# Kernel optimization log

Hardware: AMD Instinct MI355X
Metric: run time of the kernel (lower is better)

Reference implementation:

```python
import jax, jax.numpy as jnp
import numpy as np

N = 100000   # nodes
E = 1000000  # edges
D = 128      # input_dim
H = 128      # hidden_dim
P = 128      # proj_dim


def setup_inputs() -> dict:
    key = jax.random.key(0)
    ks = jax.random.split(key, 12)
    def lin(k, fi, fo):
        return jax.random.normal(k, (fi, fo), jnp.float32) / np.sqrt(fi).astype(np.float32)
    x = jax.random.normal(ks[0], (N, D), jnp.float32)
    edge_index = jax.random.randint(ks[1], (2, E), 0, N, dtype=jnp.int32)
    return {
        "x": x,
        "edge_index": edge_index,
        "W1": lin(ks[2], D, H), "b1": jnp.zeros((H,), jnp.float32),
        "W2": lin(ks[3], H, H), "b2": jnp.zeros((H,), jnp.float32),
        "Wp1": lin(ks[4], H, P), "bp1": jnp.zeros((P,), jnp.float32),
        "prelu_a": jnp.float32(0.25),
        "Wp2": lin(ks[5], P, P), "bp2": jnp.zeros((P,), jnp.float32),
    }


def _gcn_conv(h, W, b, src, dst):
    # PyG GCNConv: h' = D^{-1/2} (A + I) D^{-1/2} (h W) + b
    h = h @ W                                   # [N, H]
    loop = jnp.arange(N, dtype=src.dtype)
    s = jnp.concatenate([src, loop])            # add self-loops
    d = jnp.concatenate([dst, loop])
    deg = jax.ops.segment_sum(jnp.ones(s.shape, h.dtype), d, num_segments=N)
    dinv = jax.lax.rsqrt(jnp.maximum(deg, 1.0))  # deg >= 1 due to self-loops
    norm = dinv[s] * dinv[d]                     # [E+N]
    msg = h[s] * norm[:, None]                   # gather + scale
    return jax.ops.segment_sum(msg, d, num_segments=N) + b


def reference(x, edge_index, W1, b1, W2, b2, Wp1, bp1, prelu_a, Wp2, bp2):
    src, dst = edge_index[0], edge_index[1]
    z = jax.nn.relu(_gcn_conv(x, W1, b1, src, dst))   # dropout p=0 -> identity
    z = jax.nn.relu(_gcn_conv(z, W2, b2, src, dst))
    h = z @ Wp1 + bp1
    h = jnp.where(h > 0, h, prelu_a * h)              # PReLU
    p = h @ Wp2 + bp2
    return (z, p)
```

## Files before the change

### kernel.cpp

```cpp
#include <hip/hip_runtime.h>

typedef __bf16 bf16x8 __attribute__((ext_vector_type(8)));
typedef float  f32x4  __attribute__((ext_vector_type(4)));
typedef unsigned short us8 __attribute__((ext_vector_type(8)));
typedef unsigned short us4 __attribute__((ext_vector_type(4)));

__device__ __forceinline__ float bf2f(unsigned short u) {
    return __builtin_bit_cast(float, (unsigned int)u << 16);
}
__device__ __forceinline__ unsigned short f2bf(float f) {
    return __builtin_bit_cast(unsigned short, (__bf16)f);
}

__global__ void prep_w(const float* __restrict__ W, unsigned short* __restrict__ hiT,
                       unsigned short* __restrict__ loT) {
    int i = blockIdx.x * 256 + threadIdx.x;
    int k = i >> 7;
    int n = i & 127;
    float f = W[i];
    __bf16 h = (__bf16)f;
    __bf16 l = (__bf16)(f - (float)h);
    hiT[n * 128 + k] = __builtin_bit_cast(unsigned short, h);
    loT[n * 128 + k] = __builtin_bit_cast(unsigned short, l);
}

__global__ void to_bf16(const float* __restrict__ in, unsigned short* __restrict__ out, int n4) {
    int i = blockIdx.x * 256 + threadIdx.x;
    if (i < n4) {
        f32x4 v = ((const f32x4*)in)[i];
        us4 o;
        o[0] = f2bf(v[0]); o[1] = f2bf(v[1]); o[2] = f2bf(v[2]); o[3] = f2bf(v[3]);
        ((us4*)out)[i] = o;
    }
}

__global__ void zero_i(int* __restrict__ p, int n) {
    int i = blockIdx.x * 256 + threadIdx.x;
    if (i < n) p[i] = 0;
}

__global__ void count_deg(const int* __restrict__ dst, int* __restrict__ cnt, int E) {
    int e = blockIdx.x * 256 + threadIdx.x;
    if (e < E) atomicAdd(&cnt[dst[e]], 1);
}

__global__ void scanA(const int* __restrict__ cnt, int* __restrict__ rowptr,
                      int* __restrict__ bsum, int N) {
    __shared__ int s[1024];
    int t = threadIdx.x;
    int idx = blockIdx.x * 1024 + t;
    int v = (idx < N) ? cnt[idx] : 0;
    int sum = v;
    s[t] = sum;
    __syncthreads();
    for (int o = 1; o < 1024; o <<= 1) {
        int u = (t >= o) ? s[t - o] : 0;
        __syncthreads();
        sum += u;
        s[t] = sum;
        __syncthreads();
    }
    if (idx < N) rowptr[idx] = sum - v;
    if (t == 1023) bsum[blockIdx.x] = sum;
}

__global__ void scanB(int* __restrict__ bsum, int nb) {
    __shared__ int s[128];
    int t = threadIdx.x;
    int v = (t < nb) ? bsum[t] : 0;
    int sum = v;
    s[t] = sum;
    __syncthreads();
    for (int o = 1; o < 128; o <<= 1) {
        int u = (t >= o) ? s[t - o] : 0;
        __syncthreads();
        sum += u;
        s[t] = sum;
        __syncthreads();
    }
    if (t < nb) bsum[t] = sum - v;
}

__global__ void scanC(int* __restrict__ rowptr, const int* __restrict__ bsum,
                      int* __restrict__ cnt_cursor, float* __restrict__ dinv, int N, int E) {
    int i = blockIdx.x * 256 + threadIdx.x;
    if (i < N) {
        int c = cnt_cursor[i];
        int a = rowptr[i] + bsum[i >> 10];
        rowptr[i] = a;
        cnt_cursor[i] = a;
        dinv[i] = rsqrtf((float)(c + 1));
    }
    if (i == 0) rowptr[N] = E;
}

__global__ void fill_csr(const int* __restrict__ src, const int* __restrict__ dst,
                         int* __restrict__ cursor, int* __restrict__ colsrc, int E) {
    int e = blockIdx.x * 256 + threadIdx.x;
    if (e < E) {
        int d = dst[e];
        int p = atomicAdd(&cursor[d], 1);
        colsrc[p] = src[e];
    }
}

__global__ __launch_bounds__(256) void gemm128s(
    const unsigned short* __restrict__ Ahi, const unsigned short* __restrict__ WhiT,
    const unsigned short* __restrict__ WloT, const float* __restrict__ bias,
    const float* __restrict__ prelu_a, float* __restrict__ Cf,
    unsigned short* __restrict__ Cb, int M, int mode)
{
    __shared__ unsigned short sHi[128 * 136];
    __shared__ unsigned short sLo[128 * 136];
    const int tid = threadIdx.x;

    for (int i = tid; i < 2048; i += 256) {
        int row = i >> 4, seg = i & 15;
        *(us8*)(&sHi[row * 136 + seg * 8]) = *(const us8*)(WhiT + row * 128 + seg * 8);
        *(us8*)(&sLo[row * 136 + seg * 8]) = *(const us8*)(WloT + row * 128 + seg * 8);
    }
    __syncthreads();

    const int lane = tid & 63;
    const int wave = tid >> 6;
    const int lc   = lane & 15;
    const int quad = lane >> 4;
    const int rowBlock = blockIdx.x * 128 + wave * 32;

    f32x4 acc[2][8];
    const f32x4 z4 = {0.f, 0.f, 0.f, 0.f};
#pragma unroll
    for (int rs = 0; rs < 2; ++rs)
#pragma unroll
        for (int t = 0; t < 8; ++t) acc[rs][t] = z4;

#pragma unroll
    for (int ks = 0; ks < 4; ++ks) {
        const int kf = ks * 32 + quad * 8;
        bf16x8 a[2];
#pragma unroll
        for (int rs = 0; rs < 2; ++rs) {
            int r = rowBlock + rs * 16 + lc;
            if (r > M - 1) r = M - 1;
            a[rs] = __builtin_bit_cast(bf16x8, *(const us8*)(Ahi + (size_t)r * 128 + kf));
        }
#pragma unroll
        for (int t = 0; t < 8; ++t) {
            bf16x8 bhi = __builtin_bit_cast(bf16x8, *(const us8*)(&sHi[(t * 16 + lc) * 136 + kf]));
            bf16x8 blo = __builtin_bit_cast(bf16x8, *(const us8*)(&sLo[(t * 16 + lc) * 136 + kf]));
#pragma unroll
            for (int rs = 0; rs < 2; ++rs) {
                acc[rs][t] = __builtin_amdgcn_mfma_f32_16x16x32_bf16(a[rs], bhi, acc[rs][t], 0, 0, 0);
                acc[rs][t] = __builtin_amdgcn_mfma_f32_16x16x32_bf16(a[rs], blo, acc[rs][t], 0, 0, 0);
            }
        }
    }

    float av = (mode == 1) ? prelu_a[0] : 0.f;
#pragma unroll
    for (int t = 0; t < 8; ++t) {
        int gcol = t * 16 + lc;
        float bv = (mode != 0) ? bias[gcol] : 0.f;
#pragma unroll
        for (int rs = 0; rs < 2; ++rs) {
#pragma unroll
            for (int i = 0; i < 4; ++i) {
                int r = rowBlock + rs * 16 + quad * 4 + i;
                if (r < M) {
                    float v = acc[rs][t][i] + bv;
                    if (mode == 1) v = (v > 0.f) ? v : av * v;
                    if (mode == 2) Cf[(size_t)r * 128 + gcol] = v;
                    else           Cb[(size_t)r * 128 + gcol] = f2bf(v);
                }
            }
        }
    }
}

__global__ __launch_bounds__(128) void aggregate(
    const unsigned short* __restrict__ Hhi, const float* __restrict__ dinv,
    const int* __restrict__ rowptr, const int* __restrict__ colsrc,
    const float* __restrict__ bias, float* __restrict__ outF,
    unsigned short* __restrict__ outHi, int N)
{
    const int n = blockIdx.x;
    const int tid = threadIdx.x;
    const int g = tid >> 5;
    const int l = tid & 31;
    const float dn = dinv[n];
    const int beg = rowptr[n], end = rowptr[n + 1];

    f32x4 a0 = {0.f, 0.f, 0.f, 0.f};
    f32x4 a1 = a0;

    int i = beg + g;
    for (; i + 4 < end; i += 8) {
        int s0 = colsrc[i];
        int s1 = colsrc[i + 4];
        float w0 = dinv[s0] * dn;
        float w1 = dinv[s1] * dn;
        us4 h0 = *(const us4*)(Hhi + (size_t)s0 * 128 + l * 4);
        us4 h1 = *(const us4*)(Hhi + (size_t)s1 * 128 + l * 4);
#pragma unroll
        for (int j = 0; j < 4; ++j) a0[j] += w0 * bf2f(h0[j]);
#pragma unroll
        for (int j = 0; j < 4; ++j) a1[j] += w1 * bf2f(h1[j]);
    }
    if (i < end) {
        int s0 = colsrc[i];
        float w0 = dinv[s0] * dn;
        us4 h0 = *(const us4*)(Hhi + (size_t)s0 * 128 + l * 4);
#pragma unroll
        for (int j = 0; j < 4; ++j) a0[j] += w0 * bf2f(h0[j]);
    }

    __shared__ f32x4 red[128];
    red[tid] = a0 + a1;
    __syncthreads();

    if (tid < 32) {
        f32x4 sum = red[tid] + red[32 + tid] + red[64 + tid] + red[96 + tid];
        us4 sh = *(const us4*)(Hhi + (size_t)n * 128 + tid * 4);
        f32x4 b4 = *(const f32x4*)(bias + tid * 4);
        float ws = dn * dn;
        f32x4 v;
        us4 ob;
#pragma unroll
        for (int j = 0; j < 4; ++j) {
            v[j] = fmaxf(sum[j] + ws * bf2f(sh[j]) + b4[j], 0.f);
            ob[j] = f2bf(v[j]);
        }
        if (outF) *(f32x4*)(outF + (size_t)n * 128 + tid * 4) = v;
        *(us4*)(outHi + (size_t)n * 128 + tid * 4) = ob;
    }
}

extern "C" void kernel_launch(void* const* d_in, const int* in_sizes, int n_in,
                              void* d_out, int out_size, void* d_ws, size_t ws_size,
                              hipStream_t stream)
{
    const float* x   = (const float*)d_in[0];
    const int*   ei  = (const int*)d_in[1];
    const float* W1  = (const float*)d_in[2];
    const float* b1  = (const float*)d_in[3];
    const float* W2  = (const float*)d_in[4];
    const float* b2  = (const float*)d_in[5];
    const float* Wp1 = (const float*)d_in[6];
    const float* bp1 = (const float*)d_in[7];
    const float* pa  = (const float*)d_in[8];
    const float* Wp2 = (const float*)d_in[9];
    const float* bp2 = (const float*)d_in[10];

    const int N = in_sizes[0] / 128;
    const int E = in_sizes[1] / 2;
    const int* src = ei;
    const int* dst = ei + E;

    float* outF = (float*)d_out;
    float* zbuf = outF;
    float* pbuf = outF + (size_t)N * 128;

    char* w = (char*)d_ws;
    size_t off = 0;
    auto alloc = [&](size_t bytes) {
        void* p = w + off;
        off = (off + bytes + 255) & ~(size_t)255;
        return p;
    };
    unsigned short* S1 = (unsigned short*)alloc((size_t)N * 128 * sizeof(unsigned short));
    unsigned short* S2 = (unsigned short*)alloc((size_t)N * 128 * sizeof(unsigned short));
    float* dinv   = (float*)alloc((size_t)N * sizeof(float));
    int*   rowptr = (int*)alloc((size_t)(N + 1) * sizeof(int));
    int*   cntcur = (int*)alloc((size_t)N * sizeof(int));
    int*   colsrc = (int*)alloc((size_t)E * sizeof(int));
    int*   bsum   = (int*)alloc(1024);
    unsigned short* wt = (unsigned short*)alloc((size_t)4 * 2 * 128 * 128 * sizeof(unsigned short));
    (void)ws_size; (void)n_in; (void)out_size;

    auto hiP = [&](int m) { return wt + (size_t)m * 2 * 16384; };
    auto loP = [&](int m) { return wt + (size_t)m * 2 * 16384 + 16384; };

    hipLaunchKernelGGL(prep_w, dim3(64), dim3(256), 0, stream, W1,  hiP(0), loP(0));
    hipLaunchKernelGGL(prep_w, dim3(64), dim3(256), 0, stream, W2,  hiP(1), loP(1));
    hipLaunchKernelGGL(prep_w, dim3(64), dim3(256), 0, stream, Wp1, hiP(2), loP(2));
    hipLaunchKernelGGL(prep_w, dim3(64), dim3(256), 0, stream, Wp2, hiP(3), loP(3));

    const int n4 = N * 128 / 4;
    hipLaunchKernelGGL(to_bf16, dim3((n4 + 255) / 256), dim3(256), 0, stream, x, S1, n4);

    const int nb = (N + 1023) >> 10;
    hipLaunchKernelGGL(zero_i,    dim3((N + 255) / 256), dim3(256), 0, stream, cntcur, N);
    hipLaunchKernelGGL(count_deg, dim3((E + 255) / 256), dim3(256), 0, stream, dst, cntcur, E);
    hipLaunchKernelGGL(scanA,     dim3(nb), dim3(1024), 0, stream, cntcur, rowptr, bsum, N);
    hipLaunchKernelGGL(scanB,     dim3(1), dim3(128), 0, stream, bsum, nb);
    hipLaunchKernelGGL(scanC,     dim3((N + 255) / 256), dim3(256), 0, stream, rowptr, bsum, cntcur, dinv, N, E);
    hipLaunchKernelGGL(fill_csr,  dim3((E + 255) / 256), dim3(256), 0, stream, src, dst, cntcur, colsrc, E);

    const int gb = (N + 127) / 128;
    hipLaunchKernelGGL(gemm128s, dim3(gb), dim3(256), 0, stream, S1, hiP(0), loP(0),
                       (const float*)nullptr, (const float*)nullptr, (float*)nullptr, S2, N, 0);
    hipLaunchKernelGGL(aggregate, dim3(N), dim3(128), 0, stream, S2, dinv, rowptr, colsrc,
                       b1, (float*)nullptr, S1, N);
    hipLaunchKernelGGL(gemm128s, dim3(gb), dim3(256), 0, stream, S1, hiP(1), loP(1),
                       (const float*)nullptr, (const float*)nullptr, (float*)nullptr, S2, N, 0);
    hipLaunchKernelGGL(aggregate, dim3(N), dim3(128), 0, stream, S2, dinv, rowptr, colsrc,
                       b2, zbuf, S1, N);
    hipLaunchKernelGGL(gemm128s, dim3(gb), dim3(256), 0, stream, S1, hiP(2), loP(2),
                       bp1, pa, (float*)nullptr, S2, N, 1);
    hipLaunchKernelGGL(gemm128s, dim3(gb), dim3(256), 0, stream, S2, hiP(3), loP(3),
                       bp2, (const float*)nullptr, pbuf, (unsigned short*)nullptr, N, 2);
}
```

Before: 568.9 us.

## Pack edge weights into CSR and aggregate one warp per node

Precomputes each edge's normalization weight during CSR fill and stores it next to the source index as an int2 record, so aggregation no longer gathers dinv per edge. Aggregation now assigns one 32-lane group per destination node (8 nodes per 256-thread block) with a 4-way unrolled edge loop, removing the shared-memory reduction and the block-wide sync. It also merges the four weight-prep launches into one and replaces the zeroing kernel with a memset. In exchange the edge array doubles in size, and load balance now depends on per-node degree within a wavefront.

```diff
diff --git a/kernel.cpp b/kernel.cpp
--- a/kernel.cpp
+++ b/kernel.cpp
@@ -12,16 +12,19 @@
     return __builtin_bit_cast(unsigned short, (__bf16)f);
 }
 
-__global__ void prep_w(const float* __restrict__ W, unsigned short* __restrict__ hiT,
-                       unsigned short* __restrict__ loT) {
+__global__ void prep_w4(const float* __restrict__ W0, const float* __restrict__ W1,
+                        const float* __restrict__ W2, const float* __restrict__ W3,
+                        unsigned short* __restrict__ wt) {
     int i = blockIdx.x * 256 + threadIdx.x;
-    int k = i >> 7;
-    int n = i & 127;
-    float f = W[i];
+    int m = i >> 14, r = i & 16383;
+    const float* W = (m == 0) ? W0 : (m == 1) ? W1 : (m == 2) ? W2 : W3;
+    float f = W[r];
+    int k = r >> 7, n = r & 127;
     __bf16 h = (__bf16)f;
     __bf16 l = (__bf16)(f - (float)h);
-    hiT[n * 128 + k] = __builtin_bit_cast(unsigned short, h);
-    loT[n * 128 + k] = __builtin_bit_cast(unsigned short, l);
+    unsigned short* base = wt + m * 32768;
+    base[n * 128 + k]         = __builtin_bit_cast(unsigned short, h);
+    base[16384 + n * 128 + k] = __builtin_bit_cast(unsigned short, l);
 }
 
 __global__ void to_bf16(const float* __restrict__ in, unsigned short* __restrict__ out, int n4) {
@@ -32,11 +35,6 @@
         o[0] = f2bf(v[0]); o[1] = f2bf(v[1]); o[2] = f2bf(v[2]); o[3] = f2bf(v[3]);
         ((us4*)out)[i] = o;
     }
-}
-
-__global__ void zero_i(int* __restrict__ p, int n) {
-    int i = blockIdx.x * 256 + threadIdx.x;
-    if (i < n) p[i] = 0;
 }
 
 __global__ void count_deg(const int* __restrict__ dst, int* __restrict__ cnt, int E) {
@@ -82,25 +80,34 @@
 }
 
 __global__ void scanC(int* __restrict__ rowptr, const int* __restrict__ bsum,
-                      int* __restrict__ cnt_cursor, float* __restrict__ dinv, int N, int E) {
+                      int* __restrict__ cnt_cursor, float* __restrict__ dinv,
+                      float* __restrict__ selfw, int N, int E) {
     int i = blockIdx.x * 256 + threadIdx.x;
     if (i < N) {
         int c = cnt_cursor[i];
         int a = rowptr[i] + bsum[i >> 10];
         rowptr[i] = a;
         cnt_cursor[i] = a;
-        dinv[i] = rsqrtf((float)(c + 1));
+        float dv = rsqrtf((float)(c + 1));
+        dinv[i] = dv;
+        selfw[i] = dv * dv;
     }
     if (i == 0) rowptr[N] = E;
 }
 
 __global__ void fill_csr(const int* __restrict__ src, const int* __restrict__ dst,
-                         int* __restrict__ cursor, int* __restrict__ colsrc, int E) {
+                         int* __restrict__ cursor, const float* __restrict__ dinv,
+                         int2* __restrict__ epack, int E) {
     int e = blockIdx.x * 256 + threadIdx.x;
     if (e < E) {
+        int s = src[e];
         int d = dst[e];
+        float w = dinv[s] * dinv[d];
         int p = atomicAdd(&cursor[d], 1);
-        colsrc[p] = src[e];
+        int2 rec;
+        rec.x = s;
+        rec.y = __builtin_bit_cast(int, w);
+        epack[p] = rec;
     }
 }
 
@@ -177,62 +184,68 @@
     }
 }
 
-__global__ __launch_bounds__(128) void aggregate(
-    const unsigned short* __restrict__ Hhi, const float* __restrict__ dinv,
-    const int* __restrict__ rowptr, const int* __restrict__ colsrc,
+__global__ __launch_bounds__(256) void aggregate(
+    const unsigned short* __restrict__ Hhi, const float* __restrict__ selfw,
+    const int* __restrict__ rowptr, const int2* __restrict__ epack,
     const float* __restrict__ bias, float* __restrict__ outF,
     unsigned short* __restrict__ outHi, int N)
 {
-    const int n = blockIdx.x;
     const int tid = threadIdx.x;
     const int g = tid >> 5;
     const int l = tid & 31;
-    const float dn = dinv[n];
+    const int n = blockIdx.x * 8 + g;
+    if (n >= N) return;
+
     const int beg = rowptr[n], end = rowptr[n + 1];
+    const size_t fo = (size_t)l * 4;
 
     f32x4 a0 = {0.f, 0.f, 0.f, 0.f};
-    f32x4 a1 = a0;
-
-    int i = beg + g;
-    for (; i + 4 < end; i += 8) {
-        int s0 = colsrc[i];
-        int s1 = colsrc[i + 4];
-        float w0 = dinv[s0] * dn;
-        float w1 = dinv[s1] * dn;
-        us4 h0 = *(const us4*)(Hhi + (size_t)s0 * 128 + l * 4);
-        us4 h1 = *(const us4*)(Hhi + (size_t)s1 * 128 + l * 4);
+    f32x4 a1 = a0, a2 = a0, a3 = a0;
+
+    int i = beg;
+    for (; i + 3 < end; i += 4) {
+        int2 e0 = epack[i];
+        int2 e1 = epack[i + 1];
+        int2 e2 = epack[i + 2];
+        int2 e3 = epack[i + 3];
+        us4 h0 = *(const us4*)(Hhi + (size_t)e0.x * 128 + fo);
+        us4 h1 = *(const us4*)(Hhi + (size_t)e1.x * 128 + fo);
+        us4 h2 = *(const us4*)(Hhi + (size_t)e2.x * 128 + fo);
+        us4 h3 = *(const us4*)(Hhi + (size_t)e3.x * 128 + fo);
+        float w0 = __builtin_bit_cast(float, e0.y);
+        float w1 = __builtin_bit_cast(float, e1.y);
+        float w2 = __builtin_bit_cast(float, e2.y);
+        float w3 = __builtin_bit_cast(float, e3.y);
 #pragma unroll
         for (int j = 0; j < 4; ++j) a0[j] += w0 * bf2f(h0[j]);
 #pragma unroll
         for (int j = 0; j < 4; ++j) a1[j] += w1 * bf2f(h1[j]);
-    }
-    if (i < end) {
-        int s0 = colsrc[i];
-        float w0 = dinv[s0] * dn;
-        us4 h0 = *(const us4*)(Hhi + (size_t)s0 * 128 + l * 4);
+#pragma unroll
+        for (int j = 0; j < 4; ++j) a2[j] += w2 * bf2f(h2[j]);
+#pragma unroll
+        for (int j = 0; j < 4; ++j) a3[j] += w3 * bf2f(h3[j]);
+    }
+    for (; i < end; ++i) {
+        int2 e0 = epack[i];
+        us4 h0 = *(const us4*)(Hhi + (size_t)e0.x * 128 + fo);
+        float w0 = __builtin_bit_cast(float, e0.y);
 #pragma unroll
         for (int j = 0; j < 4; ++j) a0[j] += w0 * bf2f(h0[j]);
     }
 
-    __shared__ f32x4 red[128];
-    red[tid] = a0 + a1;
-    __syncthreads();
-
-    if (tid < 32) {
-        f32x4 sum = red[tid] + red[32 + tid] + red[64 + tid] + red[96 + tid];
-        us4 sh = *(const us4*)(Hhi + (size_t)n * 128 + tid * 4);
-        f32x4 b4 = *(const f32x4*)(bias + tid * 4);
-        float ws = dn * dn;
-        f32x4 v;
-        us4 ob;
-#pragma unroll
-        for (int j = 0; j < 4; ++j) {
-            v[j] = fmaxf(sum[j] + ws * bf2f(sh[j]) + b4[j], 0.f);
-            ob[j] = f2bf(v[j]);
-        }
-        if (outF) *(f32x4*)(outF + (size_t)n * 128 + tid * 4) = v;
-        *(us4*)(outHi + (size_t)n * 128 + tid * 4) = ob;
-    }
+    float sw = selfw[n];
+    us4 sh = *(const us4*)(Hhi + (size_t)n * 128 + fo);
+    f32x4 b4 = *(const f32x4*)(bias + l * 4);
+    f32x4 sum = (a0 + a1) + (a2 + a3);
+    f32x4 v;
+    us4 ob;
+#pragma unroll
+    for (int j = 0; j < 4; ++j) {
+        v[j] = fmaxf(sum[j] + sw * bf2f(sh[j]) + b4[j], 0.f);
+        ob[j] = f2bf(v[j]);
+    }
+    if (outF) *(f32x4*)(outF + (size_t)n * 128 + fo) = v;
+    *(us4*)(outHi + (size_t)n * 128 + fo) = ob;
 }
 
 extern "C" void kernel_launch(void* const* d_in, const int* in_sizes, int n_in,
@@ -270,40 +283,38 @@
     unsigned short* S1 = (unsigned short*)alloc((size_t)N * 128 * sizeof(unsigned short));
     unsigned short* S2 = (unsigned short*)alloc((size_t)N * 128 * sizeof(unsigned short));
     float* dinv   = (float*)alloc((size_t)N * sizeof(float));
+    float* selfw  = (float*)alloc((size_t)N * sizeof(float));
     int*   rowptr = (int*)alloc((size_t)(N + 1) * sizeof(int));
     int*   cntcur = (int*)alloc((size_t)N * sizeof(int));
-    int*   colsrc = (int*)alloc((size_t)E * sizeof(int));
+    int2*  epack  = (int2*)alloc((size_t)E * sizeof(int2));
     int*   bsum   = (int*)alloc(1024);
     unsigned short* wt = (unsigned short*)alloc((size_t)4 * 2 * 128 * 128 * sizeof(unsigned short));
     (void)ws_size; (void)n_in; (void)out_size;
 
-    auto hiP = [&](int m) { return wt + (size_t)m * 2 * 16384; };
-    auto loP = [&](int m) { return wt + (size_t)m * 2 * 16384 + 16384; };
-
-    hipLaunchKernelGGL(prep_w, dim3(64), dim3(256), 0, stream, W1,  hiP(0), loP(0));
-    hipLaunchKernelGGL(prep_w, dim3(64), dim3(256), 0, stream, W2,  hiP(1), loP(1));
-    hipLaunchKernelGGL(prep_w, dim3(64), dim3(256), 0, stream, Wp1, hiP(2), loP(2));
-    hipLaunchKernelGGL(prep_w, dim3(64), dim3(256), 0, stream, Wp2, hiP(3), loP(3));
-
+    auto hiP = [&](int m) { return wt + (size_t)m * 32768; };
+    auto loP = [&](int m) { return wt + (size_t)m * 32768 + 16384; };
+
+    hipLaunchKernelGGL(prep_w4, dim3(256), dim3(256), 0, stream, W1, W2, Wp1, Wp2, wt);
     const int n4 = N * 128 / 4;
     hipLaunchKernelGGL(to_bf16, dim3((n4 + 255) / 256), dim3(256), 0, stream, x, S1, n4);
 
+    hipMemsetAsync(cntcur, 0, (size_t)N * sizeof(int), stream);
     const int nb = (N + 1023) >> 10;
-    hipLaunchKernelGGL(zero_i,    dim3((N + 255) / 256), dim3(256), 0, stream, cntcur, N);
     hipLaunchKernelGGL(count_deg, dim3((E + 255) / 256), dim3(256), 0, stream, dst, cntcur, E);
     hipLaunchKernelGGL(scanA,     dim3(nb), dim3(1024), 0, stream, cntcur, rowptr, bsum, N);
     hipLaunchKernelGGL(scanB,     dim3(1), dim3(128), 0, stream, bsum, nb);
-    hipLaunchKernelGGL(scanC,     dim3((N + 255) / 256), dim3(256), 0, stream, rowptr, bsum, cntcur, dinv, N, E);
-    hipLaunchKernelGGL(fill_csr,  dim3((E + 255) / 256), dim3(256), 0, stream, src, dst, cntcur, colsrc, E);
+    hipLaunchKernelGGL(scanC,     dim3((N + 255) / 256), dim3(256), 0, stream, rowptr, bsum, cntcur, dinv, selfw, N, E);
+    hipLaunchKernelGGL(fill_csr,  dim3((E + 255) / 256), dim3(256), 0, stream, src, dst, cntcur, dinv, epack, E);
 
     const int gb = (N + 127) / 128;
+    const int ab = (N + 7) / 8;
     hipLaunchKernelGGL(gemm128s, dim3(gb), dim3(256), 0, stream, S1, hiP(0), loP(0),
                        (const float*)nullptr, (const float*)nullptr, (float*)nullptr, S2, N, 0);
-    hipLaunchKernelGGL(aggregate, dim3(N), dim3(128), 0, stream, S2, dinv, rowptr, colsrc,
+    hipLaunchKernelGGL(aggregate, dim3(ab), dim3(256), 0, stream, S2, selfw, rowptr, epack,
                        b1, (float*)nullptr, S1, N);
     hipLaunchKernelGGL(gemm128s, dim3(gb), dim3(256), 0, stream, S1, hiP(1), loP(1),
                        (const float*)nullptr, (const float*)nullptr, (float*)nullptr, S2, N, 0);
-    hipLaunchKernelGGL(aggregate, dim3(N), dim3(128), 0, stream, S2, dinv, rowptr, colsrc,
+    hipLaunchKernelGGL(aggregate, dim3(ab), dim3(256), 0, stream, S2, selfw, rowptr, epack,
                        b2, zbuf, S1, N);
     hipLaunchKernelGGL(gemm128s, dim3(gb), dim3(256), 0, stream, S1, hiP(2), loP(2),
                        bp1, pa, (float*)nullptr, S2, N, 1);
```

New measurement: 493.0 us. 1.15x faster.
